# Kernel optimization log

Measured on AMD Instinct MI355X. Metric: run time of the kernel, lower is better.

## Reference

```python
import jax, jax.numpy as jnp
import numpy as np

D = 128          # embedding_dim
H = 8            # attention heads
DH = D // H      # per-head dim
SPLIT = 50000    # hyper-edge zero rows prepended
NX = 150000      # input node feature rows
N0 = SPLIT + NX  # layer-0 source nodes
N1 = 50000       # layer-0 targets
N2 = 30000       # layer-1 targets
N3 = 10000       # layer-2 targets
E0, E1, E2 = 500000, 300000, 100000
NTYPE = 65       # e_num + 1 edge types
NEG_SLOPE = 0.2
BETA = 0.5       # residual_beta (learn_beta=False)
BN_EPS = 1e-5

WEIGHT_NAMES = ['Wq0','Wk0','Wv0','Ws0','Wq1','Wk1','Wv1','Ws1','Wek1','Wev1','Wq2','Wk2','Wv2','Ws2']


def setup_inputs() -> dict:
    key = jax.random.key(0)
    ks = jax.random.split(key, 32)
    s = 1.0 / np.sqrt(D)
    inp = {}
    inp['x'] = jax.random.normal(ks[0], (NX, D), jnp.float32)
    inp['type_table'] = jax.random.normal(ks[1], (NTYPE, D), jnp.float32) * s
    inp['attr_table'] = jax.random.normal(ks[2], (NTYPE, D), jnp.float32) * s
    for i, nm in enumerate(WEIGHT_NAMES):
        inp[nm] = jax.random.normal(ks[3 + i], (D, D), jnp.float32) * s
    inp['g0'] = jnp.ones((D,), jnp.float32)
    inp['b0'] = jnp.zeros((D,), jnp.float32)
    inp['src0'] = jax.random.randint(ks[20], (E0,), 0, N0)
    inp['dst0'] = jax.random.randint(ks[21], (E0,), 0, N1)
    inp['src1'] = jax.random.randint(ks[22], (E1,), 0, N1)
    inp['dst1'] = jax.random.randint(ks[23], (E1,), 0, N2)
    inp['src2'] = jax.random.randint(ks[24], (E2,), 0, N2)
    inp['dst2'] = jax.random.randint(ks[25], (E2,), 0, N3)
    inp['edge_type'] = jax.random.randint(ks[26], (E1,), 0, NTYPE)
    return inp


def _conv(x_src, x_tgt, src, dst, Wq, Wk, Wv, Ws, ek=None, ev=None):
    # HypergraphTransformer: multi-head attention over incoming edges per target.
    Nt = x_tgt.shape[0]
    q = (x_tgt @ Wq).reshape(Nt, H, DH)
    k = (x_src @ Wk)[src]            # [E, D] project at nodes, gather at edges
    v = (x_src @ Wv)[src]
    if ek is not None:
        k = k + ek
        v = v + ev
    k = k.reshape(-1, H, DH)
    v = v.reshape(-1, H, DH)
    logits = (q[dst] * k).sum(-1) / np.sqrt(DH)          # [E, H]
    logits = jnp.where(logits >= 0, logits, NEG_SLOPE * logits)
    m = jax.ops.segment_max(logits, dst, num_segments=Nt)
    m = jnp.where(jnp.isfinite(m), m, 0.0)
    a = jnp.exp(logits - m[dst])
    ssum = jax.ops.segment_sum(a, dst, num_segments=Nt)
    alpha = a / (ssum[dst] + 1e-16)                      # segment softmax
    out = jax.ops.segment_sum(alpha[..., None] * v, dst, num_segments=Nt)
    out = out.reshape(Nt, D)                             # concat head fusion
    return BETA * (x_tgt @ Ws) + (1.0 - BETA) * out      # gated residual


def _bn(h, g, b):
    mu = h.mean(0)
    var = h.var(0)   # biased, as torch BatchNorm1d uses for normalization in training
    return (h - mu) / jnp.sqrt(var + BN_EPS) * g + b


def reference(x, type_table, attr_table, Wq0, Wk0, Wv0, Ws0, Wq1, Wk1, Wv1, Ws1,
              Wek1, Wev1, Wq2, Wk2, Wv2, Ws2, g0, b0,
              src0, dst0, src1, dst1, src2, dst2, edge_type):
    # prepend split_idx zero rows for hyper-edge embeddings
    h = jnp.concatenate([jnp.zeros((SPLIT, D), x.dtype), x], axis=0)  # [N0, D]
    # idx 0: v2e + BatchNorm
    h = _conv(h, h[:N1], src0, dst0, Wq0, Wk0, Wv0, Ws0)
    h = _bn(h, g0, b0)
    # idx 1: E2EConvs[0] with edge_type/attr embeddings added to K/V
    ek = type_table[edge_type] @ Wek1
    ev = attr_table[edge_type] @ Wev1
    h = _conv(h, h[:N2], src1, dst1, Wq1, Wk1, Wv1, Ws1, ek=ek, ev=ev)
    # idx 2: e2rel (no edge embeddings)
    h = _conv(h, h[:N3], src2, dst2, Wq2, Wk2, Wv2, Ws2)
    return h
```

## Files before the change

kernel.cpp:

```cpp
#include <hip/hip_runtime.h>
#include <math.h>

#define DD 128
#define SPLIT 50000
#define NN1 50000
#define NN2 30000
#define NN3 10000
#define EE0 500000
#define EE1 300000
#define EE2 100000
#define EALL (EE0 + EE1 + EE2)
#define NALL (NN1 + NN2 + NN3)
#define B1 50000
#define B2 80000
#define NEG 0.2f

__global__ __launch_bounds__(256) void hist_kernel(
    const int* __restrict__ dst0, const int* __restrict__ dst1,
    const int* __restrict__ dst2, int* __restrict__ counts)
{
  for (int e = blockIdx.x * 256 + threadIdx.x; e < EALL; e += gridDim.x * 256) {
    int d;
    if (e < EE0) d = dst0[e];
    else if (e < EE0 + EE1) d = B1 + dst1[e - EE0];
    else d = B2 + dst2[e - EE0 - EE1];
    atomicAdd(&counts[d], 1);
  }
}

__global__ __launch_bounds__(256) void scan1_kernel(
    const int* __restrict__ counts, int* __restrict__ rp1,
    int* __restrict__ partial, int n)
{
  __shared__ int s[256];
  int t = threadIdx.x;
  int i = blockIdx.x * 256 + t;
  int v = (i < n) ? counts[i] : 0;
  s[t] = v; __syncthreads();
  for (int off = 1; off < 256; off <<= 1) {
    int tv = (t >= off) ? s[t - off] : 0;
    __syncthreads();
    s[t] += tv;
    __syncthreads();
  }
  if (i < n) rp1[i] = s[t];
  if (t == 255) partial[blockIdx.x] = s[255];
}

__global__ __launch_bounds__(256) void scan2_kernel(int* __restrict__ partial, int nb)
{
  __shared__ int s[256];
  int t = threadIdx.x;
  int carry = 0;
  for (int base = 0; base < nb; base += 256) {
    int i = base + t;
    int v = (i < nb) ? partial[i] : 0;
    s[t] = v; __syncthreads();
    for (int off = 1; off < 256; off <<= 1) {
      int tv = (t >= off) ? s[t - off] : 0;
      __syncthreads();
      s[t] += tv;
      __syncthreads();
    }
    int ex = carry + ((t == 0) ? 0 : s[t - 1]);
    if (i < nb) partial[i] = ex;
    int tot = s[255];
    __syncthreads();
    carry += tot;
  }
}

__global__ __launch_bounds__(256) void scan3_kernel(
    int* __restrict__ rp, const int* __restrict__ partial, int n)
{
  int i = blockIdx.x * 256 + threadIdx.x;
  if (i < n) rp[i + 1] += partial[i >> 8];
  if (i == 0) rp[0] = 0;
}

__global__ __launch_bounds__(256) void fill_kernel(
    const int* __restrict__ dst0, const int* __restrict__ src0,
    const int* __restrict__ dst1, const int* __restrict__ src1,
    const int* __restrict__ dst2, const int* __restrict__ src2,
    const int* __restrict__ etyp, int* __restrict__ cursor,
    int* __restrict__ vals)
{
  for (int e = blockIdx.x * 256 + threadIdx.x; e < EALL; e += gridDim.x * 256) {
    int d, v;
    if (e < EE0) { d = dst0[e]; v = src0[e]; }
    else if (e < EE0 + EE1) {
      int k = e - EE0;
      d = B1 + dst1[k]; v = src1[k] | (etyp[k] << 17);
    } else {
      int k = e - EE0 - EE1;
      d = B2 + dst2[k]; v = src2[k];
    }
    int slot = atomicAdd(&cursor[d], 1);
    vals[slot] = v;
  }
}

__global__ __launch_bounds__(256) void agg0_kernel(
    const float* __restrict__ x, const int* __restrict__ rp,
    const int* __restrict__ vals, float* __restrict__ acc, float* __restrict__ deg)
{
  int d = blockIdx.x * 4 + (threadIdx.x >> 6);
  if (d >= NN1) return;
  int lane = threadIdx.x & 63;
  int l32 = lane & 31, half = lane >> 5;
  int beg = rp[d], end = rp[d + 1];
  const float4* x4 = (const float4*)x;
  float4 a0 = {0.f, 0.f, 0.f, 0.f}, a1 = {0.f, 0.f, 0.f, 0.f};
  int j = beg + half;
  for (; j + 2 < end; j += 4) {
    int s0 = vals[j], s1 = vals[j + 2];
    if (s0 >= SPLIT) {
      float4 v = x4[(size_t)(s0 - SPLIT) * 32 + l32];
      a0.x += v.x; a0.y += v.y; a0.z += v.z; a0.w += v.w;
    }
    if (s1 >= SPLIT) {
      float4 v = x4[(size_t)(s1 - SPLIT) * 32 + l32];
      a1.x += v.x; a1.y += v.y; a1.z += v.z; a1.w += v.w;
    }
  }
  if (j < end) {
    int s0 = vals[j];
    if (s0 >= SPLIT) {
      float4 v = x4[(size_t)(s0 - SPLIT) * 32 + l32];
      a0.x += v.x; a0.y += v.y; a0.z += v.z; a0.w += v.w;
    }
  }
  a0.x += a1.x; a0.y += a1.y; a0.z += a1.z; a0.w += a1.w;
  a0.x += __shfl(a0.x, l32 + 32);
  a0.y += __shfl(a0.y, l32 + 32);
  a0.z += __shfl(a0.z, l32 + 32);
  a0.w += __shfl(a0.w, l32 + 32);
  if (half == 0) {
    ((float4*)acc)[(size_t)d * 32 + l32] = a0;
    if (l32 == 0) deg[d] = (float)(end - beg);
  }
}

__global__ __launch_bounds__(256) void gemm128_kernel(
    const float* __restrict__ A, const float* __restrict__ W,
    float* __restrict__ C, int N, const float* __restrict__ deg)
{
  __shared__ float Al[64 * 128];
  __shared__ float Wl[64 * 128];
  int t = threadIdx.x;
  int cg = t & 31;
  int rg = t >> 5;
  int r0 = blockIdx.x << 6;
  int nrows = N - r0; if (nrows > 64) nrows = 64;

  const float4* Ag = (const float4*)(A + (size_t)r0 * DD);
  float4* Al4 = (float4*)Al;
  for (int i = t; i < nrows * 32; i += 256) Al4[i] = Ag[i];

  float acc[8][4] = {};
  const float4* W4 = (const float4*)W;
  float4* Wl4 = (float4*)Wl;
  const float4* Al4c = (const float4*)Al;

  for (int half = 0; half < 2; ++half) {
    __syncthreads();
    for (int i = t; i < 2048; i += 256) Wl4[i] = W4[half * 2048 + i];
    __syncthreads();
    const float4* Wl4c = (const float4*)Wl;
    int kb4 = half * 16;
    for (int k4 = 0; k4 < 16; ++k4) {
      float4 w0 = Wl4c[(k4 * 4 + 0) * 32 + cg];
      float4 w1 = Wl4c[(k4 * 4 + 1) * 32 + cg];
      float4 w2 = Wl4c[(k4 * 4 + 2) * 32 + cg];
      float4 w3 = Wl4c[(k4 * 4 + 3) * 32 + cg];
#pragma unroll
      for (int r = 0; r < 8; ++r) {
        float4 a = Al4c[(rg * 8 + r) * 32 + kb4 + k4];
        acc[r][0] = fmaf(a.x, w0.x, acc[r][0]);
        acc[r][1] = fmaf(a.x, w0.y, acc[r][1]);
        acc[r][2] = fmaf(a.x, w0.z, acc[r][2]);
        acc[r][3] = fmaf(a.x, w0.w, acc[r][3]);
        acc[r][0] = fmaf(a.y, w1.x, acc[r][0]);
        acc[r][1] = fmaf(a.y, w1.y, acc[r][1]);
        acc[r][2] = fmaf(a.y, w1.z, acc[r][2]);
        acc[r][3] = fmaf(a.y, w1.w, acc[r][3]);
        acc[r][0] = fmaf(a.z, w2.x, acc[r][0]);
        acc[r][1] = fmaf(a.z, w2.y, acc[r][1]);
        acc[r][2] = fmaf(a.z, w2.z, acc[r][2]);
        acc[r][3] = fmaf(a.z, w2.w, acc[r][3]);
        acc[r][0] = fmaf(a.w, w3.x, acc[r][0]);
        acc[r][1] = fmaf(a.w, w3.y, acc[r][1]);
        acc[r][2] = fmaf(a.w, w3.z, acc[r][2]);
        acc[r][3] = fmaf(a.w, w3.w, acc[r][3]);
      }
    }
  }

#pragma unroll
  for (int r = 0; r < 8; ++r) {
    int rr = rg * 8 + r;
    if (rr < nrows) {
      float sc = 1.0f;
      if (deg) sc = 0.5f / (deg[r0 + rr] + 1e-16f);
      float4 o;
      o.x = acc[r][0] * sc; o.y = acc[r][1] * sc;
      o.z = acc[r][2] * sc; o.w = acc[r][3] * sc;
      ((float4*)(C + (size_t)(r0 + rr) * DD))[cg] = o;
    }
  }
}

__global__ __launch_bounds__(256) void gemm4_kernel(
    const float* __restrict__ A, const float* __restrict__ SC,
    const float* __restrict__ SH,
    const float* __restrict__ W0, float* __restrict__ C0, int N0,
    const float* __restrict__ W1, float* __restrict__ C1, int N1,
    const float* __restrict__ W2, float* __restrict__ C2, int N2,
    const float* __restrict__ W3, float* __restrict__ C3, int N3)
{
  __shared__ float Al[64 * 128];
  __shared__ float Wl[64 * 128];
  int t = threadIdx.x;
  int cg = t & 31;
  int rg = t >> 5;
  int r0 = blockIdx.x << 6;
  int nrows = N0 - r0; if (nrows > 64) nrows = 64;

  const float4* Ag = (const float4*)(A + (size_t)r0 * DD);
  float4* Al4 = (float4*)Al;
  if (SC) {
    const float4* SC4 = (const float4*)SC;
    const float4* SH4 = (const float4*)SH;
    for (int i = t; i < nrows * 32; i += 256) {
      float4 a = Ag[i];
      float4 sc = SC4[i & 31], sh = SH4[i & 31];
      a.x = fmaf(a.x, sc.x, sh.x);
      a.y = fmaf(a.y, sc.y, sh.y);
      a.z = fmaf(a.z, sc.z, sh.z);
      a.w = fmaf(a.w, sc.w, sh.w);
      Al4[i] = a;
    }
  } else {
    for (int i = t; i < nrows * 32; i += 256) Al4[i] = Ag[i];
  }

  const float* Ws[4] = {W0, W1, W2, W3};
  float* Cs[4] = {C0, C1, C2, C3};
  int Ns[4] = {N0, N1, N2, N3};
  const float4* Al4c = (const float4*)Al;
  float4* Wl4 = (float4*)Wl;

#pragma unroll
  for (int o = 0; o < 4; ++o) {
    if (r0 >= Ns[o]) continue;
    int nr = Ns[o] - r0; if (nr > 64) nr = 64;
    float acc[8][4] = {};
    const float4* W4 = (const float4*)Ws[o];
    for (int half = 0; half < 2; ++half) {
      __syncthreads();
      for (int i = t; i < 2048; i += 256) Wl4[i] = W4[half * 2048 + i];
      __syncthreads();
      const float4* Wl4c = (const float4*)Wl;
      int kb4 = half * 16;
      for (int k4 = 0; k4 < 16; ++k4) {
        float4 w0 = Wl4c[(k4 * 4 + 0) * 32 + cg];
        float4 w1 = Wl4c[(k4 * 4 + 1) * 32 + cg];
        float4 w2 = Wl4c[(k4 * 4 + 2) * 32 + cg];
        float4 w3 = Wl4c[(k4 * 4 + 3) * 32 + cg];
#pragma unroll
        for (int r = 0; r < 8; ++r) {
          float4 a = Al4c[(rg * 8 + r) * 32 + kb4 + k4];
          acc[r][0] = fmaf(a.x, w0.x, acc[r][0]);
          acc[r][1] = fmaf(a.x, w0.y, acc[r][1]);
          acc[r][2] = fmaf(a.x, w0.z, acc[r][2]);
          acc[r][3] = fmaf(a.x, w0.w, acc[r][3]);
          acc[r][0] = fmaf(a.y, w1.x, acc[r][0]);
          acc[r][1] = fmaf(a.y, w1.y, acc[r][1]);
          acc[r][2] = fmaf(a.y, w1.z, acc[r][2]);
          acc[r][3] = fmaf(a.y, w1.w, acc[r][3]);
          acc[r][0] = fmaf(a.z, w2.x, acc[r][0]);
          acc[r][1] = fmaf(a.z, w2.y, acc[r][1]);
          acc[r][2] = fmaf(a.z, w2.z, acc[r][2]);
          acc[r][3] = fmaf(a.z, w2.w, acc[r][3]);
          acc[r][0] = fmaf(a.w, w3.x, acc[r][0]);
          acc[r][1] = fmaf(a.w, w3.y, acc[r][1]);
          acc[r][2] = fmaf(a.w, w3.z, acc[r][2]);
          acc[r][3] = fmaf(a.w, w3.w, acc[r][3]);
        }
      }
    }
#pragma unroll
    for (int r = 0; r < 8; ++r) {
      int rr = rg * 8 + r;
      if (rr < nr) {
        float4 ov;
        ov.x = acc[r][0]; ov.y = acc[r][1]; ov.z = acc[r][2]; ov.w = acc[r][3];
        ((float4*)(Cs[o] + (size_t)(r0 + rr) * DD))[cg] = ov;
      }
    }
  }
}

__global__ __launch_bounds__(256) void bn_stats_kernel(
    const float* __restrict__ H, float* __restrict__ sums)
{
  int t = threadIdx.x;
  int col = t & 127;
  float s = 0.f, q = 0.f;
  for (int r = blockIdx.x * 2 + (t >> 7); r < NN1; r += gridDim.x * 2) {
    float v = H[(size_t)r * DD + col];
    s += v; q += v * v;
  }
  __shared__ float ls[256], lq[256];
  ls[t] = s; lq[t] = q;
  __syncthreads();
  if (t < 128) {
    atomicAdd(&sums[col], ls[t] + ls[t + 128]);
    atomicAdd(&sums[128 + col], lq[t] + lq[t + 128]);
  }
}

__global__ __launch_bounds__(128) void bn_finalize_kernel(
    const float* __restrict__ sums, const float* __restrict__ g,
    const float* __restrict__ b, float* __restrict__ SC, float* __restrict__ SH)
{
  int c = threadIdx.x;
  const float invN = 1.0f / (float)NN1;
  float mu = sums[c] * invN;
  float var = sums[128 + c] * invN - mu * mu;
  float rs = rsqrtf(var + 1e-5f);
  float sc = rs * g[c];
  SC[c] = sc;
  SH[c] = b[c] - mu * sc;
}

__global__ __launch_bounds__(256) void attn_kernel(
    const float* __restrict__ Q, const float* __restrict__ K,
    const float* __restrict__ V, const float* __restrict__ EKT,
    const float* __restrict__ EVT, const int* __restrict__ rp,
    const int* __restrict__ vals, const float* __restrict__ Spre,
    float* __restrict__ Out, int Nt)
{
  int d = blockIdx.x * 4 + (threadIdx.x >> 6);
  if (d >= Nt) return;
  int lane = threadIdx.x & 63;
  int l32 = lane & 31, half = lane >> 5;

  const float4* Q4 = (const float4*)Q;
  const float4* K4 = (const float4*)K;
  const float4* V4 = (const float4*)V;
  float4 q = Q4[(size_t)d * 32 + l32];

  float m = -INFINITY, ss = 0.f;
  float4 o = {0.f, 0.f, 0.f, 0.f};

  int beg = rp[d], end = rp[d + 1];
  for (int j = beg + half; j < end; j += 2) {
    int pv = vals[j];
    float4 kk, vv;
    if (EKT) {
      int s = pv & 0x1FFFF, ty = pv >> 17;
      kk = K4[(size_t)s * 32 + l32];
      vv = V4[(size_t)s * 32 + l32];
      float4 ek = ((const float4*)EKT)[(size_t)ty * 32 + l32];
      float4 ev = ((const float4*)EVT)[(size_t)ty * 32 + l32];
      kk.x += ek.x; kk.y += ek.y; kk.z += ek.z; kk.w += ek.w;
      vv.x += ev.x; vv.y += ev.y; vv.z += ev.z; vv.w += ev.w;
    } else {
      kk = K4[(size_t)pv * 32 + l32];
      vv = V4[(size_t)pv * 32 + l32];
    }
    float p = q.x * kk.x + q.y * kk.y + q.z * kk.z + q.w * kk.w;
    p += __shfl_xor(p, 1);
    p += __shfl_xor(p, 2);
    float l = p * 0.25f;
    l = (l >= 0.f) ? l : NEG * l;
    float nm = fmaxf(m, l);
    float w = __expf(m - nm);
    float a = __expf(l - nm);
    ss = ss * w + a;
    o.x = o.x * w + a * vv.x;
    o.y = o.y * w + a * vv.y;
    o.z = o.z * w + a * vv.z;
    o.w = o.w * w + a * vv.w;
    m = nm;
  }

  float mp = __shfl_xor(m, 32);
  float sp = __shfl_xor(ss, 32);
  float4 op;
  op.x = __shfl_xor(o.x, 32);
  op.y = __shfl_xor(o.y, 32);
  op.z = __shfl_xor(o.z, 32);
  op.w = __shfl_xor(o.w, 32);
  float nm = fmaxf(m, mp);
  if (nm == -INFINITY) nm = 0.f;
  float w = __expf(m - nm);
  float wp = __expf(mp - nm);
  float sT = ss * w + sp * wp;
  float inv = 1.0f / (sT + 1e-16f);
  float4 res;
  res.x = (o.x * w + op.x * wp) * inv;
  res.y = (o.y * w + op.y * wp) * inv;
  res.z = (o.z * w + op.z * wp) * inv;
  res.w = (o.w * w + op.w * wp) * inv;

  if (half == 0) {
    float4 sr = ((const float4*)Spre)[(size_t)d * 32 + l32];
    float4 ot;
    ot.x = 0.5f * (sr.x + res.x);
    ot.y = 0.5f * (sr.y + res.y);
    ot.z = 0.5f * (sr.z + res.z);
    ot.w = 0.5f * (sr.w + res.w);
    ((float4*)Out)[(size_t)d * 32 + l32] = ot;
  }
}

extern "C" void kernel_launch(void* const* d_in, const int* in_sizes, int n_in,
                              void* d_out, int out_size, void* d_ws, size_t ws_size,
                              hipStream_t stream)
{
  const float* x   = (const float*)d_in[0];
  const float* tt  = (const float*)d_in[1];
  const float* at  = (const float*)d_in[2];
  const float* Wv0 = (const float*)d_in[5];
  const float* Wq1 = (const float*)d_in[7];
  const float* Wk1 = (const float*)d_in[8];
  const float* Wv1 = (const float*)d_in[9];
  const float* Ws1 = (const float*)d_in[10];
  const float* Wek1= (const float*)d_in[11];
  const float* Wev1= (const float*)d_in[12];
  const float* Wq2 = (const float*)d_in[13];
  const float* Wk2 = (const float*)d_in[14];
  const float* Wv2 = (const float*)d_in[15];
  const float* Ws2 = (const float*)d_in[16];
  const float* g0  = (const float*)d_in[17];
  const float* b0  = (const float*)d_in[18];
  const int* src0 = (const int*)d_in[19];
  const int* dst0 = (const int*)d_in[20];
  const int* src1 = (const int*)d_in[21];
  const int* dst1 = (const int*)d_in[22];
  const int* src2 = (const int*)d_in[23];
  const int* dst2 = (const int*)d_in[24];
  const int* etyp = (const int*)d_in[25];

  float* ws = (float*)d_ws;

  const size_t O_K1  = 0;
  const size_t O_V1  = 6400000;
  const size_t O_Q1  = 12800000;
  const size_t O_H2  = 16640000;
  const size_t O_DEG = 20480000;
  const size_t O_EK  = 20530000;
  const size_t O_EV  = 20538320;
  const size_t O_BN  = 20546640;
  const size_t O_SC  = 20546896;
  const size_t O_SH  = 20547024;
  const size_t O_H1  = 20547152;
  const size_t O_K2  = 0;
  const size_t O_V2  = 3840000;
  const size_t O_Q2  = 7680000;
  const size_t O_S2  = 8960000;
  int* wi   = (int*)(ws + 26947152);
  int* RP   = wi;
  int* VALS = wi + 90001;
  int* CNT  = wi + 990001;
  int* PART = wi + 1080001;

  hipMemsetAsync(CNT, 0, (size_t)NALL * 4, stream);
  hist_kernel<<<3516, 256, 0, stream>>>(dst0, dst1, dst2, CNT);
  int nb = (NALL + 255) / 256;
  scan1_kernel<<<nb, 256, 0, stream>>>(CNT, RP + 1, PART, NALL);
  scan2_kernel<<<1, 256, 0, stream>>>(PART, nb);
  scan3_kernel<<<nb, 256, 0, stream>>>(RP, PART, NALL);
  hipMemcpyAsync(CNT, RP, (size_t)NALL * 4, hipMemcpyDeviceToDevice, stream);
  fill_kernel<<<3516, 256, 0, stream>>>(dst0, src0, dst1, src1, dst2, src2,
                                        etyp, CNT, VALS);

  hipMemsetAsync(ws + O_BN, 0, (size_t)256 * 4, stream);

  agg0_kernel<<<(NN1 + 3) / 4, 256, 0, stream>>>(x, RP, VALS, ws + O_K1, ws + O_DEG);
  gemm128_kernel<<<(NN1 + 63) / 64, 256, 0, stream>>>(ws + O_K1, Wv0, ws + O_H1, NN1, ws + O_DEG);
  bn_stats_kernel<<<512, 256, 0, stream>>>(ws + O_H1, ws + O_BN);
  bn_finalize_kernel<<<1, 128, 0, stream>>>(ws + O_BN, g0, b0, ws + O_SC, ws + O_SH);

  gemm4_kernel<<<(NN1 + 63) / 64, 256, 0, stream>>>(
      ws + O_H1, ws + O_SC, ws + O_SH,
      Wk1, ws + O_K1, NN1,
      Wv1, ws + O_V1, NN1,
      Wq1, ws + O_Q1, NN2,
      Ws1, ws + O_H2, NN2);
  gemm128_kernel<<<2, 256, 0, stream>>>(tt, Wek1, ws + O_EK, 65, nullptr);
  gemm128_kernel<<<2, 256, 0, stream>>>(at, Wev1, ws + O_EV, 65, nullptr);

  attn_kernel<<<(NN2 + 3) / 4, 256, 0, stream>>>(
      ws + O_Q1, ws + O_K1, ws + O_V1, ws + O_EK, ws + O_EV,
      RP + B1, VALS, ws + O_H2, ws + O_H2, NN2);

  gemm4_kernel<<<(NN2 + 63) / 64, 256, 0, stream>>>(
      ws + O_H2, nullptr, nullptr,
      Wk2, ws + O_K2, NN2,
      Wv2, ws + O_V2, NN2,
      Wq2, ws + O_Q2, NN3,
      Ws2, ws + O_S2, NN3);

  attn_kernel<<<(NN3 + 3) / 4, 256, 0, stream>>>(
      ws + O_Q2, ws + O_K2, ws + O_V2, nullptr, nullptr,
      RP + B2, VALS, ws + O_S2, (float*)d_out, NN3);

  (void)in_sizes; (void)n_in; (void)out_size; (void)ws_size;
}
```

Before: 600.3 us.

## Replace FP32 SIMT GEMMs with split-bf16 MFMA GEMMs using pre-transposed weights

The dense 128x128 projections now run on MFMA bf16 instructions instead of scalar FMA loops with LDS tiling. Each fp32 value is split into a bf16 high part and a bf16 low part, and three MFMAs per tile approximate fp32 accuracy. A new prep kernel converts and transposes the nine weight matrices on every call. The aim is to cut the ALU-bound GEMM time, at the cost of an extra small kernel, direct global weight loads with no LDS staging, and a slight loss of precision.

```diff
diff --git a/kernel.cpp b/kernel.cpp
--- a/kernel.cpp
+++ b/kernel.cpp
@@ -15,6 +15,18 @@
 #define B2 80000
 #define NEG 0.2f
 
+typedef __attribute__((ext_vector_type(8))) short bf16x8;
+typedef __attribute__((ext_vector_type(4))) float f32x4;
+
+static __device__ __forceinline__ unsigned short f2bf(float x) {
+  unsigned u = __float_as_uint(x);
+  unsigned r = (u + 0x7FFFu + ((u >> 16) & 1u)) >> 16;
+  return (unsigned short)r;
+}
+static __device__ __forceinline__ float bf2f(unsigned short b) {
+  return __uint_as_float(((unsigned)b) << 16);
+}
+
 __global__ __launch_bounds__(256) void hist_kernel(
     const int* __restrict__ dst0, const int* __restrict__ dst1,
     const int* __restrict__ dst2, int* __restrict__ counts)
@@ -97,6 +109,22 @@
     }
     int slot = atomicAdd(&cursor[d], 1);
     vals[slot] = v;
+  }
+}
+
+struct W9 { const float* w[9]; };
+__global__ __launch_bounds__(256) void wprep_kernel(W9 srcs, unsigned short* out)
+{
+  int m = blockIdx.y;
+  const float* W = srcs.w[m];
+  unsigned short* hi = out + (size_t)m * 32768;
+  unsigned short* lo = hi + 16384;
+  for (int i = blockIdx.x * 256 + threadIdx.x; i < 16384; i += gridDim.x * 256) {
+    int k = i >> 7, c = i & 127;
+    float a = W[i];
+    unsigned short h = f2bf(a);
+    hi[c * DD + k] = h;
+    lo[c * DD + k] = f2bf(a - bf2f(h));
   }
 }
 
@@ -210,95 +238,96 @@
   }
 }
 
-__global__ __launch_bounds__(256) void gemm4_kernel(
-    const float* __restrict__ A, const float* __restrict__ SC,
-    const float* __restrict__ SH,
-    const float* __restrict__ W0, float* __restrict__ C0, int N0,
-    const float* __restrict__ W1, float* __restrict__ C1, int N1,
-    const float* __restrict__ W2, float* __restrict__ C2, int N2,
-    const float* __restrict__ W3, float* __restrict__ C3, int N3)
-{
-  __shared__ float Al[64 * 128];
-  __shared__ float Wl[64 * 128];
+__global__ __launch_bounds__(256) void mfma_gemm4_kernel(
+    const float* __restrict__ A,
+    const float* __restrict__ SC, const float* __restrict__ SH,
+    const unsigned short* __restrict__ WP,
+    int w0, int w1, int w2, int w3,
+    float* __restrict__ C0, float* __restrict__ C1,
+    float* __restrict__ C2, float* __restrict__ C3,
+    int N0, int N1, int N2, int N3,
+    const float* __restrict__ deg)
+{
   int t = threadIdx.x;
-  int cg = t & 31;
-  int rg = t >> 5;
+  int l = t & 63;
+  int wl = t >> 6;
   int r0 = blockIdx.x << 6;
-  int nrows = N0 - r0; if (nrows > 64) nrows = 64;
-
-  const float4* Ag = (const float4*)(A + (size_t)r0 * DD);
-  float4* Al4 = (float4*)Al;
-  if (SC) {
-    const float4* SC4 = (const float4*)SC;
-    const float4* SH4 = (const float4*)SH;
-    for (int i = t; i < nrows * 32; i += 256) {
-      float4 a = Ag[i];
-      float4 sc = SC4[i & 31], sh = SH4[i & 31];
-      a.x = fmaf(a.x, sc.x, sh.x);
-      a.y = fmaf(a.y, sc.y, sh.y);
-      a.z = fmaf(a.z, sc.z, sh.z);
-      a.w = fmaf(a.w, sc.w, sh.w);
-      Al4[i] = a;
-    }
-  } else {
-    for (int i = t; i < nrows * 32; i += 256) Al4[i] = Ag[i];
-  }
-
-  const float* Ws[4] = {W0, W1, W2, W3};
-  float* Cs[4] = {C0, C1, C2, C3};
-  int Ns[4] = {N0, N1, N2, N3};
-  const float4* Al4c = (const float4*)Al;
-  float4* Wl4 = (float4*)Wl;
-
-#pragma unroll
-  for (int o = 0; o < 4; ++o) {
-    if (r0 >= Ns[o]) continue;
-    int nr = Ns[o] - r0; if (nr > 64) nr = 64;
-    float acc[8][4] = {};
-    const float4* W4 = (const float4*)Ws[o];
-    for (int half = 0; half < 2; ++half) {
-      __syncthreads();
-      for (int i = t; i < 2048; i += 256) Wl4[i] = W4[half * 2048 + i];
-      __syncthreads();
-      const float4* Wl4c = (const float4*)Wl;
-      int kb4 = half * 16;
-      for (int k4 = 0; k4 < 16; ++k4) {
-        float4 w0 = Wl4c[(k4 * 4 + 0) * 32 + cg];
-        float4 w1 = Wl4c[(k4 * 4 + 1) * 32 + cg];
-        float4 w2 = Wl4c[(k4 * 4 + 2) * 32 + cg];
-        float4 w3 = Wl4c[(k4 * 4 + 3) * 32 + cg];
-#pragma unroll
-        for (int r = 0; r < 8; ++r) {
-          float4 a = Al4c[(rg * 8 + r) * 32 + kb4 + k4];
-          acc[r][0] = fmaf(a.x, w0.x, acc[r][0]);
-          acc[r][1] = fmaf(a.x, w0.y, acc[r][1]);
-          acc[r][2] = fmaf(a.x, w0.z, acc[r][2]);
-          acc[r][3] = fmaf(a.x, w0.w, acc[r][3]);
-          acc[r][0] = fmaf(a.y, w1.x, acc[r][0]);
-          acc[r][1] = fmaf(a.y, w1.y, acc[r][1]);
-          acc[r][2] = fmaf(a.y, w1.z, acc[r][2]);
-          acc[r][3] = fmaf(a.y, w1.w, acc[r][3]);
-          acc[r][0] = fmaf(a.z, w2.x, acc[r][0]);
-          acc[r][1] = fmaf(a.z, w2.y, acc[r][1]);
-          acc[r][2] = fmaf(a.z, w2.z, acc[r][2]);
-          acc[r][3] = fmaf(a.z, w2.w, acc[r][3]);
-          acc[r][0] = fmaf(a.w, w3.x, acc[r][0]);
-          acc[r][1] = fmaf(a.w, w3.y, acc[r][1]);
-          acc[r][2] = fmaf(a.w, w3.z, acc[r][2]);
-          acc[r][3] = fmaf(a.w, w3.w, acc[r][3]);
-        }
+  int rbase = r0 + wl * 16 + (l & 15);
+  int r_ld = rbase < N0 ? rbase : (N0 - 1);
+  int kg = (l >> 4) << 3;
+
+  bf16x8 Ah[4], Al[4];
+#pragma unroll
+  for (int ks = 0; ks < 4; ++ks) {
+    int k0 = ks * 32 + kg;
+    const float4* ap = (const float4*)(A + (size_t)r_ld * DD + k0);
+    float4 x0 = ap[0], x1 = ap[1];
+    float av[8] = {x0.x, x0.y, x0.z, x0.w, x1.x, x1.y, x1.z, x1.w};
+    if (SC) {
+      const float4* scp = (const float4*)(SC + k0);
+      const float4* shp = (const float4*)(SH + k0);
+      float4 s0 = scp[0], s1 = scp[1], h0 = shp[0], h1 = shp[1];
+      av[0] = fmaf(av[0], s0.x, h0.x);
+      av[1] = fmaf(av[1], s0.y, h0.y);
+      av[2] = fmaf(av[2], s0.z, h0.z);
+      av[3] = fmaf(av[3], s0.w, h0.w);
+      av[4] = fmaf(av[4], s1.x, h1.x);
+      av[5] = fmaf(av[5], s1.y, h1.y);
+      av[6] = fmaf(av[6], s1.z, h1.z);
+      av[7] = fmaf(av[7], s1.w, h1.w);
+    }
+#pragma unroll
+    for (int j = 0; j < 8; ++j) {
+      unsigned short h = f2bf(av[j]);
+      Ah[ks][j] = (short)h;
+      Al[ks][j] = (short)f2bf(av[j] - bf2f(h));
+    }
+  }
+
+  auto do_out = [&](int widx, float* C, int N, bool useDeg) {
+    if (widx < 0 || r0 >= N) return;
+    const unsigned short* Wh = WP + (size_t)widx * 32768;
+    const unsigned short* Wl = Wh + 16384;
+    f32x4 acc[8];
+#pragma unroll
+    for (int ct = 0; ct < 8; ++ct) acc[ct] = (f32x4){0.f, 0.f, 0.f, 0.f};
+#pragma unroll
+    for (int ks = 0; ks < 4; ++ks) {
+      int koff = ks * 32 + kg;
+#pragma unroll
+      for (int ct = 0; ct < 8; ++ct) {
+        int col = ct * 16 + (l & 15);
+        bf16x8 bh = *(const bf16x8*)(Wh + (size_t)col * DD + koff);
+        bf16x8 bl = *(const bf16x8*)(Wl + (size_t)col * DD + koff);
+        acc[ct] = __builtin_amdgcn_mfma_f32_16x16x32_bf16(Ah[ks], bh, acc[ct], 0, 0, 0);
+        acc[ct] = __builtin_amdgcn_mfma_f32_16x16x32_bf16(Al[ks], bh, acc[ct], 0, 0, 0);
+        acc[ct] = __builtin_amdgcn_mfma_f32_16x16x32_bf16(Ah[ks], bl, acc[ct], 0, 0, 0);
       }
     }
-#pragma unroll
-    for (int r = 0; r < 8; ++r) {
-      int rr = rg * 8 + r;
-      if (rr < nr) {
-        float4 ov;
-        ov.x = acc[r][0]; ov.y = acc[r][1]; ov.z = acc[r][2]; ov.w = acc[r][3];
-        ((float4*)(Cs[o] + (size_t)(r0 + rr) * DD))[cg] = ov;
+    int rw = r0 + wl * 16 + ((l >> 4) << 2);
+    float scl[4] = {1.f, 1.f, 1.f, 1.f};
+    if (useDeg) {
+#pragma unroll
+      for (int r = 0; r < 4; ++r) {
+        int rr = rw + r; if (rr > N - 1) rr = N - 1;
+        scl[r] = 0.5f / (deg[rr] + 1e-16f);
       }
     }
-  }
+#pragma unroll
+    for (int ct = 0; ct < 8; ++ct) {
+      int col = ct * 16 + (l & 15);
+#pragma unroll
+      for (int r = 0; r < 4; ++r) {
+        int row = rw + r;
+        if (row < N) C[(size_t)row * DD + col] = acc[ct][r] * scl[r];
+      }
+    }
+  };
+
+  do_out(w0, C0, N0, deg != nullptr);
+  do_out(w1, C1, N1, false);
+  do_out(w2, C2, N2, false);
+  do_out(w3, C3, N3, false);
 }
 
 __global__ __launch_bounds__(256) void bn_stats_kernel(
@@ -373,11 +402,11 @@
     float p = q.x * kk.x + q.y * kk.y + q.z * kk.z + q.w * kk.w;
     p += __shfl_xor(p, 1);
     p += __shfl_xor(p, 2);
-    float l = p * 0.25f;
-    l = (l >= 0.f) ? l : NEG * l;
-    float nm = fmaxf(m, l);
+    float lg = p * 0.25f;
+    lg = (lg >= 0.f) ? lg : NEG * lg;
+    float nm = fmaxf(m, lg);
     float w = __expf(m - nm);
-    float a = __expf(l - nm);
+    float a = __expf(lg - nm);
     ss = ss * w + a;
     o.x = o.x * w + a * vv.x;
     o.y = o.y * w + a * vv.y;
@@ -466,6 +495,13 @@
   int* VALS = wi + 90001;
   int* CNT  = wi + 990001;
   int* PART = wi + 1080001;
+  unsigned short* WPREP = (unsigned short*)(wi + 1080520);
+
+  W9 w9;
+  w9.w[0] = Wv0;
+  w9.w[1] = Wk1; w9.w[2] = Wv1; w9.w[3] = Wq1; w9.w[4] = Ws1;
+  w9.w[5] = Wk2; w9.w[6] = Wv2; w9.w[7] = Wq2; w9.w[8] = Ws2;
+  wprep_kernel<<<dim3(8, 9), 256, 0, stream>>>(w9, WPREP);
 
   hipMemsetAsync(CNT, 0, (size_t)NALL * 4, stream);
   hist_kernel<<<3516, 256, 0, stream>>>(dst0, dst1, dst2, CNT);
@@ -480,16 +516,19 @@
   hipMemsetAsync(ws + O_BN, 0, (size_t)256 * 4, stream);
 
   agg0_kernel<<<(NN1 + 3) / 4, 256, 0, stream>>>(x, RP, VALS, ws + O_K1, ws + O_DEG);
-  gemm128_kernel<<<(NN1 + 63) / 64, 256, 0, stream>>>(ws + O_K1, Wv0, ws + O_H1, NN1, ws + O_DEG);
+  mfma_gemm4_kernel<<<(NN1 + 63) / 64, 256, 0, stream>>>(
+      ws + O_K1, nullptr, nullptr, WPREP,
+      0, -1, -1, -1,
+      ws + O_H1, nullptr, nullptr, nullptr,
+      NN1, 0, 0, 0, ws + O_DEG);
   bn_stats_kernel<<<512, 256, 0, stream>>>(ws + O_H1, ws + O_BN);
   bn_finalize_kernel<<<1, 128, 0, stream>>>(ws + O_BN, g0, b0, ws + O_SC, ws + O_SH);
 
-  gemm4_kernel<<<(NN1 + 63) / 64, 256, 0, stream>>>(
-      ws + O_H1, ws + O_SC, ws + O_SH,
-      Wk1, ws + O_K1, NN1,
-      Wv1, ws + O_V1, NN1,
-      Wq1, ws + O_Q1, NN2,
-      Ws1, ws + O_H2, NN2);
+  mfma_gemm4_kernel<<<(NN1 + 63) / 64, 256, 0, stream>>>(
+      ws + O_H1, ws + O_SC, ws + O_SH, WPREP,
+      1, 2, 3, 4,
+      ws + O_K1, ws + O_V1, ws + O_Q1, ws + O_H2,
+      NN1, NN1, NN2, NN2, nullptr);
   gemm128_kernel<<<2, 256, 0, stream>>>(tt, Wek1, ws + O_EK, 65, nullptr);
   gemm128_kernel<<<2, 256, 0, stream>>>(at, Wev1, ws + O_EV, 65, nullptr);
 
@@ -497,12 +536,11 @@
       ws + O_Q1, ws + O_K1, ws + O_V1, ws + O_EK, ws + O_EV,
       RP + B1, VALS, ws + O_H2, ws + O_H2, NN2);
 
-  gemm4_kernel<<<(NN2 + 63) / 64, 256, 0, stream>>>(
-      ws + O_H2, nullptr, nullptr,
-      Wk2, ws + O_K2, NN2,
-      Wv2, ws + O_V2, NN2,
-      Wq2, ws + O_Q2, NN3,
-      Ws2, ws + O_S2, NN3);
+  mfma_gemm4_kernel<<<(NN2 + 63) / 64, 256, 0, stream>>>(
+      ws + O_H2, nullptr, nullptr, WPREP,
+      5, 6, 7, 8,
+      ws + O_K2, ws + O_V2, ws + O_Q2, ws + O_S2,
+      NN2, NN2, NN3, NN3, nullptr);
 
   attn_kernel<<<(NN3 + 3) / 4, 256, 0, stream>>>(
       ws + O_Q2, ws + O_K2, ws + O_V2, nullptr, nullptr,
```

Result: no change. 606.8 us (+1.1%).
